# Kernel optimization log

Measured on AMD Instinct MI355X. Metric: run time of the kernel, lower is better.

The kernel has to match this reference:

```python
import jax, jax.numpy as jnp
import numpy as np

B, T, D, H, FF = 4, 2048, 1024, 16, 4096
HD = D // H
EPS = 1e-5


def setup_inputs() -> dict:
    key = jax.random.key(0)
    ks = jax.random.split(key, 10)
    s = lambda k, shape, fan: jax.random.normal(k, shape, jnp.float32) * (1.0 / np.sqrt(fan))
    return {
        "x": jax.random.normal(ks[0], (B, T, D), jnp.float32),
        "ln1_g": jnp.ones((D,), jnp.float32),
        "ln1_b": jnp.zeros((D,), jnp.float32),
        "qkv_w": s(ks[1], (D, 3 * D), D),
        "qkv_b": jnp.zeros((3 * D,), jnp.float32),
        "proj_w": s(ks[2], (D, D), D),
        "proj_b": jnp.zeros((D,), jnp.float32),
        "ln2_g": jnp.ones((D,), jnp.float32),
        "ln2_b": jnp.zeros((D,), jnp.float32),
        "ff1_w": s(ks[3], (D, FF), D),
        "ff1_b": jnp.zeros((FF,), jnp.float32),
        "ff2_w": s(ks[4], (FF, D), FF),
        "ff2_b": jnp.zeros((D,), jnp.float32),
    }


def _layernorm(x, g, b):
    mu = jnp.mean(x, axis=-1, keepdims=True)
    var = jnp.mean(jnp.square(x - mu), axis=-1, keepdims=True)
    return (x - mu) * jax.lax.rsqrt(var + EPS) * g + b


def reference(x, ln1_g, ln1_b, qkv_w, qkv_b, proj_w, proj_b,
              ln2_g, ln2_b, ff1_w, ff1_b, ff2_w, ff2_b):
    # --- attention sublayer ---
    h = _layernorm(x, ln1_g, ln1_b)
    qkv = h @ qkv_w + qkv_b                      # [B,T,3D]
    q, k, v = jnp.split(qkv, 3, axis=-1)
    q = q.reshape(B, T, H, HD).transpose(0, 2, 1, 3)  # [B,H,T,hd]
    k = k.reshape(B, T, H, HD).transpose(0, 2, 1, 3)
    v = v.reshape(B, T, H, HD).transpose(0, 2, 1, 3)
    att = jnp.einsum('bhqd,bhkd->bhqk', q, k) / np.sqrt(HD)
    causal = jnp.tril(jnp.ones((T, T), bool))
    att = jnp.where(causal, att, jnp.finfo(att.dtype).min)
    att = jax.nn.softmax(att, axis=-1)
    out = jnp.einsum('bhqk,bhkd->bhqd', att, v)  # [B,H,T,hd]
    out = out.transpose(0, 2, 1, 3).reshape(B, T, D)
    x = x + out @ proj_w + proj_b
    # --- MLP sublayer ---
    h = _layernorm(x, ln2_g, ln2_b)
    h = jax.nn.gelu(h @ ff1_w + ff1_b, approximate=True)
    x = x + h @ ff2_w + ff2_b
    return x
```

## Files before the change

kernel.cpp:

```cpp
#include <hip/hip_runtime.h>

typedef __attribute__((ext_vector_type(4))) float f32x4;
typedef __attribute__((ext_vector_type(8))) short s16x8;
typedef __attribute__((ext_vector_type(4))) unsigned short u16x4;

#define DEV __device__ __forceinline__

DEV unsigned short f2bf(float f) {
  unsigned int u = __float_as_uint(f);
  return (unsigned short)((u + 0x7FFFu + ((u >> 16) & 1u)) >> 16);
}

DEV float exp2_asm(float x) {
  float r; asm("v_exp_f32 %0, %1" : "=v"(r) : "v"(x)); return r;
}
DEV float rcp_asm(float x) {
  float r; asm("v_rcp_f32 %0, %1" : "=v"(r) : "v"(x)); return r;
}

DEV void gload_lds16(const void* g, void* l) {
  __builtin_amdgcn_global_load_lds(
      (const __attribute__((address_space(1))) unsigned int*)g,
      (__attribute__((address_space(3))) unsigned int*)l, 16, 0, 0);
}

__global__ __launch_bounds__(256) void ln_kernel(
    const float* __restrict__ x, const float* __restrict__ gam,
    const float* __restrict__ bet, unsigned short* __restrict__ o)
{
  const int row = blockIdx.x;
  const int tid = threadIdx.x;
  f32x4 v = *(const f32x4*)(x + (size_t)row * 1024 + tid * 4);
  float s = v[0] + v[1] + v[2] + v[3];
  float s2 = v[0]*v[0] + v[1]*v[1] + v[2]*v[2] + v[3]*v[3];
  #pragma unroll
  for (int m = 1; m < 64; m <<= 1) { s += __shfl_xor(s, m); s2 += __shfl_xor(s2, m); }
  __shared__ float ps[4], ps2[4];
  const int wid = tid >> 6, lane = tid & 63;
  if (lane == 0) { ps[wid] = s; ps2[wid] = s2; }
  __syncthreads();
  s = ps[0] + ps[1] + ps[2] + ps[3];
  s2 = ps2[0] + ps2[1] + ps2[2] + ps2[3];
  const float mu = s * (1.0f / 1024.0f);
  const float rstd = rsqrtf(s2 * (1.0f / 1024.0f) - mu * mu + 1e-5f);
  f32x4 g4 = *(const f32x4*)(gam + tid * 4);
  f32x4 b4 = *(const f32x4*)(bet + tid * 4);
  u16x4 ov;
  #pragma unroll
  for (int j = 0; j < 4; j++) ov[j] = f2bf((v[j] - mu) * rstd * g4[j] + b4[j]);
  *(u16x4*)(o + (size_t)row * 1024 + tid * 4) = ov;
}

__global__ __launch_bounds__(256) void transpose_kernel(
    const float* __restrict__ W, unsigned short* __restrict__ WT, int K, int N)
{
  __shared__ float tile[64][65];
  const int n0 = blockIdx.x * 64, k0 = blockIdx.y * 64;
  const int c = threadIdx.x & 63, r0 = threadIdx.x >> 6;
  #pragma unroll
  for (int r = r0; r < 64; r += 4)
    tile[r][c] = W[(size_t)(k0 + r) * N + n0 + c];
  __syncthreads();
  #pragma unroll
  for (int r = r0; r < 64; r += 4)
    WT[(size_t)(n0 + r) * K + k0 + c] = f2bf(tile[c][r]);
}

template <int MODE>
__global__ __launch_bounds__(512) void gemm8_kernel(
    const unsigned short* __restrict__ A, const unsigned short* __restrict__ WT,
    const float* __restrict__ bias, const float* resid, void* outp,
    int M, int N, int K)
{
  __shared__ unsigned short lds[3 * 24576];
  const int tid = threadIdx.x;
  const int lane = tid & 63, wid = tid >> 6;
  const int l15 = lane & 15, l4 = lane >> 4;
  const int wm = wid >> 2, wn = wid & 3;
  const int tiles_n = N >> 8;
  const int cpx = gridDim.x >> 3;
  const int id = (blockIdx.x & 7) * cpx + (blockIdx.x >> 3);
  const int bm = id / tiles_n, bn = id % tiles_n;
  const int NT = K >> 6;

  const int srow = tid >> 3;
  const int scol = ((tid & 7) ^ (srow & 7)) * 8;
  const unsigned short* Asrc = A  + (size_t)(bm * 128 + srow) * K + scol;
  const unsigned short* Bsrc = WT + (size_t)(bn * 256 + srow) * K + scol;
  const size_t j64 = (size_t)64 * K;
  const int dwave = wid * 1024;

#define STAGE(t_, ss_) do { \
    char* base_ = (char*)lds + (ss_) * 49152 + dwave; \
    const unsigned short* sA_ = Asrc + (size_t)(t_) * 64; \
    const unsigned short* sB_ = Bsrc + (size_t)(t_) * 64; \
    gload_lds16(sA_,            base_); \
    gload_lds16(sA_ + j64,      base_ + 8192); \
    gload_lds16(sB_,            base_ + 16384); \
    gload_lds16(sB_ + j64,      base_ + 16384 + 8192); \
    gload_lds16(sB_ + 2 * j64,  base_ + 16384 + 16384); \
    gload_lds16(sB_ + 3 * j64,  base_ + 16384 + 24576); \
  } while (0)

  f32x4 acc[4][4] = {};

  const int arow0 = wm * 64 + l15;
  const int brow0 = wn * 64 + l15;
  const int cswz = l15 & 7;

  STAGE(0, 0);
  STAGE(1, 1);
  asm volatile("s_waitcnt vmcnt(6)" ::: "memory");
  __builtin_amdgcn_s_barrier();

  int cs = 0, ss = 2;
  for (int t = 0; t < NT; ++t) {
    const unsigned short* sa = lds + cs * 24576;
    const unsigned short* sb = sa + 8192;
    s16x8 af[4][2], bf[4][2];
    #pragma unroll
    for (int mf = 0; mf < 4; ++mf)
      #pragma unroll
      for (int ks = 0; ks < 2; ++ks)
        af[mf][ks] = *(const s16x8*)&sa[(arow0 + mf * 16) * 64 + (((ks * 4 + l4) ^ cswz) * 8)];
    #pragma unroll
    for (int nf = 0; nf < 4; ++nf)
      #pragma unroll
      for (int ks = 0; ks < 2; ++ks)
        bf[nf][ks] = *(const s16x8*)&sb[(brow0 + nf * 16) * 64 + (((ks * 4 + l4) ^ cswz) * 8)];
    if (t + 2 < NT) STAGE(t + 2, ss);
    __builtin_amdgcn_s_setprio(1);
    #pragma unroll
    for (int mf = 0; mf < 4; ++mf)
      #pragma unroll
      for (int nf = 0; nf < 4; ++nf)
        #pragma unroll
        for (int ks = 0; ks < 2; ++ks)
          acc[mf][nf] = __builtin_amdgcn_mfma_f32_16x16x32_bf16(
              af[mf][ks], bf[nf][ks], acc[mf][nf], 0, 0, 0);
    __builtin_amdgcn_s_setprio(0);
    if (t + 2 < NT)      { asm volatile("s_waitcnt vmcnt(6)" ::: "memory"); }
    else if (t + 1 < NT) { asm volatile("s_waitcnt vmcnt(0)" ::: "memory"); }
    __builtin_amdgcn_s_barrier();
    cs = (cs == 2) ? 0 : cs + 1;
    ss = (ss == 2) ? 0 : ss + 1;
  }
#undef STAGE

  #pragma unroll
  for (int nf = 0; nf < 4; nf++) {
    const int col = bn * 256 + wn * 64 + nf * 16 + l15;
    const float bv = bias[col];
    #pragma unroll
    for (int mf = 0; mf < 4; mf++) {
      #pragma unroll
      for (int r = 0; r < 4; r++) {
        const int row = bm * 128 + wm * 64 + mf * 16 + l4 * 4 + r;
        const size_t off = (size_t)row * N + col;
        float v = acc[mf][nf][r] + bv;
        if (MODE == 1) {
          ((float*)outp)[off] = v + resid[off];
        } else if (MODE == 2) {
          const float u = v + 0.044715f * v * v * v;
          const float e = exp2_asm(-2.3022010f * u);
          ((unsigned short*)outp)[off] = f2bf(v * rcp_asm(1.0f + e));
        } else {
          ((unsigned short*)outp)[off] = f2bf(v);
        }
      }
    }
  }
}

struct AttnState {
  f32x4 o[4];
  float m, l;
};

DEV void attn_tile(const s16x8* qf, const unsigned short* Ks,
                   const unsigned short* Vt, unsigned short* Pw,
                   AttnState& st, int kv0, int qg, int l15, int l4, bool need_mask)
{
  f32x4 sa[4];
  #pragma unroll
  for (int cb = 0; cb < 4; cb++) sa[cb] = (f32x4){0.f, 0.f, 0.f, 0.f};
  __builtin_amdgcn_s_setprio(1);
  #pragma unroll
  for (int ks = 0; ks < 2; ++ks) {
    #pragma unroll
    for (int cb = 0; cb < 4; cb++) {
      const int kvr = cb * 16 + l15;
      s16x8 bk = *(const s16x8*)&Ks[kvr * 64 + ((ks * 32 + l4 * 8) ^ ((kvr & 7) << 3))];
      sa[cb] = __builtin_amdgcn_mfma_f32_16x16x32_bf16(bk, qf[ks], sa[cb], 0, 0, 0);
    }
  }
  __builtin_amdgcn_s_setprio(0);
  float mx = -3.0e38f;
  const int thr = qg - kv0 - l4 * 4;
  #pragma unroll
  for (int cb = 0; cb < 4; cb++)
    #pragma unroll
    for (int r = 0; r < 4; r++) {
      float sv = sa[cb][r] * 0.18033688f;
      if (need_mask && (cb * 16 + r > thr)) sv = -3.0e38f;
      sa[cb][r] = sv;
      mx = fmaxf(mx, sv);
    }
  mx = fmaxf(mx, __shfl_xor(mx, 16));
  mx = fmaxf(mx, __shfl_xor(mx, 32));
  const bool skip = __all(mx <= st.m + 11.5f);
  const float mnew = skip ? st.m : fmaxf(st.m, mx);
  float rsum = 0.f;
  #pragma unroll
  for (int cb = 0; cb < 4; cb++) {
    u16x4 pw;
    #pragma unroll
    for (int r = 0; r < 4; r++) {
      const float p = exp2_asm(sa[cb][r] - mnew);
      rsum += p;
      pw[r] = f2bf(p);
    }
    *(u16x4*)&Pw[l15 * 64 + ((cb * 16 + l4 * 4) ^ ((l15 & 7) << 3))] = pw;
  }
  rsum += __shfl_xor(rsum, 16);
  rsum += __shfl_xor(rsum, 32);
  if (skip) {
    st.l += rsum;
  } else {
    const float alpha = exp2_asm(st.m - mnew);
    st.l = st.l * alpha + rsum;
    st.m = mnew;
    #pragma unroll
    for (int r = 0; r < 4; r++) {
      const float ar = __shfl(alpha, l4 * 4 + r);
      #pragma unroll
      for (int cb = 0; cb < 4; cb++) st.o[cb][r] *= ar;
    }
  }
  asm volatile("s_waitcnt lgkmcnt(0)" ::: "memory");
  __builtin_amdgcn_s_setprio(1);
  #pragma unroll
  for (int ks = 0; ks < 2; ++ks) {
    s16x8 pa = *(const s16x8*)&Pw[l15 * 64 + ((ks * 32 + l4 * 8) ^ ((l15 & 7) << 3))];
    #pragma unroll
    for (int cb = 0; cb < 4; cb++) {
      const int d = cb * 16 + l15;
      s16x8 vf = *(const s16x8*)&Vt[d * 64 + ((ks * 32 + l4 * 8) ^ (((d >> 2) & 7) << 3))];
      st.o[cb] = __builtin_amdgcn_mfma_f32_16x16x32_bf16(pa, vf, st.o[cb], 0, 0, 0);
    }
  }
  __builtin_amdgcn_s_setprio(0);
}

DEV void attn_write(unsigned short* orow, const AttnState& st, int l15, int l4) {
  const float invl = rcp_asm(st.l);
  #pragma unroll
  for (int r = 0; r < 4; r++) {
    const float ir = __shfl(invl, l4 * 4 + r);
    #pragma unroll
    for (int cb = 0; cb < 4; cb++)
      orow[(l4 * 4 + r) * 1024 + cb * 16 + l15] = f2bf(st.o[cb][r] * ir);
  }
}

__global__ __launch_bounds__(256) void attn_kernel(
    const unsigned short* __restrict__ qkv, unsigned short* __restrict__ outb)
{
  __shared__ unsigned short Ks[2][64 * 64];
  __shared__ unsigned short Vt[64 * 64];
  __shared__ unsigned short Ps[2][4][16 * 64];
  const int pid = blockIdx.x;
  const int qA = pid, qB = 31 - pid;
  const int bh = blockIdx.y;
  const int b = bh >> 4, h = bh & 15;
  const int tid = threadIdx.x, lane = tid & 63, wid = tid >> 6;
  const int l15 = lane & 15, l4 = lane >> 4;
  const size_t base = (size_t)b * 2048 * 3072 + (size_t)h * 64;
  const unsigned short* Qb = qkv + base;
  const unsigned short* Kb = qkv + base + 1024;
  const unsigned short* Vb = qkv + base + 2048;

  s16x8 qfA[2], qfB[2];
  {
    const unsigned short* qr = Qb + (size_t)(qA * 64 + wid * 16 + l15) * 3072 + l4 * 8;
    qfA[0] = *(const s16x8*)qr;
    qfA[1] = *(const s16x8*)(qr + 32);
    qr = Qb + (size_t)(qB * 64 + wid * 16 + l15) * 3072 + l4 * 8;
    qfB[0] = *(const s16x8*)qr;
    qfB[1] = *(const s16x8*)(qr + 32);
  }

  u16x4 vv[4];
  #pragma unroll
  for (int it = 0; it < 4; ++it) {
    const int cc = tid + 256 * it;
    vv[it] = *(const u16x4*)(Vb + (size_t)(cc >> 4) * 3072 + (cc & 15) * 4);
  }
  #pragma unroll
  for (int s = 0; s < 2; ++s) {
    const int c = s * 256 + tid;
    const int kv = c >> 3;
    const int dsrc = ((c & 7) * 8) ^ ((kv & 7) << 3);
    gload_lds16(Kb + (size_t)kv * 3072 + dsrc, &Ks[0][(size_t)(c & ~63) * 8]);
  }

  AttnState sA, sB;
  #pragma unroll
  for (int cb = 0; cb < 4; cb++) {
    sA.o[cb] = (f32x4){0.f, 0.f, 0.f, 0.f};
    sB.o[cb] = (f32x4){0.f, 0.f, 0.f, 0.f};
  }
  sA.m = -1e30f; sA.l = 0.f; sB.m = -1e30f; sB.l = 0.f;
  const int qgA = qA * 64 + wid * 16 + l15;
  const int qgB = qB * 64 + wid * 16 + l15;

  for (int kvb = 0; kvb <= qB; ++kvb) {
    const int cur = kvb & 1;
    const int kv0 = kvb * 64;
    __builtin_amdgcn_s_barrier();
    asm volatile("s_waitcnt vmcnt(2)" ::: "memory");
    #pragma unroll
    for (int it = 0; it < 4; ++it) {
      const int cc = tid + 256 * it;
      const int vkv = cc >> 4;
      const int vd = (cc & 15) * 4;
      #pragma unroll
      for (int j = 0; j < 4; j++) {
        const int d = vd + j;
        Vt[d * 64 + (vkv ^ (((d >> 2) & 7) << 3))] = vv[it][j];
      }
    }
    if (kvb < qB) {
      #pragma unroll
      for (int it = 0; it < 4; ++it) {
        const int cc = tid + 256 * it;
        vv[it] = *(const u16x4*)(Vb + (size_t)((kvb + 1) * 64 + (cc >> 4)) * 3072 + (cc & 15) * 4);
      }
      asm volatile("s_waitcnt vmcnt(4)" ::: "memory");
    } else {
      asm volatile("s_waitcnt vmcnt(0)" ::: "memory");
    }
    asm volatile("s_waitcnt lgkmcnt(0)" ::: "memory");
    __builtin_amdgcn_s_barrier();
    if (kvb < qB) {
      #pragma unroll
      for (int s = 0; s < 2; ++s) {
        const int c = s * 256 + tid;
        const int kv = c >> 3;
        const int dsrc = ((c & 7) * 8) ^ ((kv & 7) << 3);
        gload_lds16(Kb + (size_t)((kvb + 1) * 64 + kv) * 3072 + dsrc,
                    &Ks[cur ^ 1][(size_t)(c & ~63) * 8]);
      }
    }
    if (kvb <= qA)
      attn_tile(qfA, Ks[cur], Vt, Ps[0][wid], sA, kv0, qgA, l15, l4,
                kv0 + 63 > qA * 64 + wid * 16);
    attn_tile(qfB, Ks[cur], Vt, Ps[1][wid], sB, kv0, qgB, l15, l4,
              kv0 + 63 > qB * 64 + wid * 16);
  }
  attn_write(outb + ((size_t)b * 2048 + qA * 64 + wid * 16) * 1024 + h * 64, sA, l15, l4);
  attn_write(outb + ((size_t)b * 2048 + qB * 64 + wid * 16) * 1024 + h * 64, sB, l15, l4);
}

extern "C" void kernel_launch(void* const* d_in, const int* in_sizes, int n_in,
                              void* d_out, int out_size, void* d_ws, size_t ws_size,
                              hipStream_t stream) {
  const float* x      = (const float*)d_in[0];
  const float* ln1_g  = (const float*)d_in[1];
  const float* ln1_b  = (const float*)d_in[2];
  const float* qkv_w  = (const float*)d_in[3];
  const float* qkv_b  = (const float*)d_in[4];
  const float* proj_w = (const float*)d_in[5];
  const float* proj_b = (const float*)d_in[6];
  const float* ln2_g  = (const float*)d_in[7];
  const float* ln2_b  = (const float*)d_in[8];
  const float* ff1_w  = (const float*)d_in[9];
  const float* ff1_b  = (const float*)d_in[10];
  const float* ff2_w  = (const float*)d_in[11];
  const float* ff2_b  = (const float*)d_in[12];
  float* out = (float*)d_out;

  char* ws = (char*)d_ws;
  size_t off = 0;
  unsigned short* wbuf   = (unsigned short*)(ws + off); off += (size_t)4096 * 1024 * 2;
  unsigned short* hbuf   = (unsigned short*)(ws + off); off += (size_t)8192 * 1024 * 2;
  unsigned short* qkvbuf = (unsigned short*)(ws + off); off += (size_t)8192 * 3072 * 2;
  unsigned short* gbuf   = (unsigned short*)(ws + off);

  ln_kernel<<<8192, 256, 0, stream>>>(x, ln1_g, ln1_b, hbuf);
  transpose_kernel<<<dim3(3072 / 64, 1024 / 64), 256, 0, stream>>>(qkv_w, wbuf, 1024, 3072);
  gemm8_kernel<0><<<dim3(64 * 12), 512, 0, stream>>>(hbuf, wbuf, qkv_b, nullptr, qkvbuf,
                                                     8192, 3072, 1024);
  attn_kernel<<<dim3(16, 64), 256, 0, stream>>>(qkvbuf, hbuf);
  transpose_kernel<<<dim3(1024 / 64, 1024 / 64), 256, 0, stream>>>(proj_w, wbuf, 1024, 1024);
  gemm8_kernel<1><<<dim3(64 * 4), 512, 0, stream>>>(hbuf, wbuf, proj_b, x, out,
                                                    8192, 1024, 1024);
  ln_kernel<<<8192, 256, 0, stream>>>(out, ln2_g, ln2_b, hbuf);
  transpose_kernel<<<dim3(4096 / 64, 1024 / 64), 256, 0, stream>>>(ff1_w, wbuf, 1024, 4096);
  gemm8_kernel<2><<<dim3(64 * 16), 512, 0, stream>>>(hbuf, wbuf, ff1_b, nullptr, gbuf,
                                                     8192, 4096, 1024);
  transpose_kernel<<<dim3(1024 / 64, 4096 / 64), 256, 0, stream>>>(ff2_w, wbuf, 4096, 1024);
  gemm8_kernel<1><<<dim3(64 * 4), 512, 0, stream>>>(gbuf, wbuf, ff2_b, out, out,
                                                    8192, 1024, 4096);
}
```

Measured before the change: 455.1 us.

## Fuse paired query-tile attention to share K/V LDS fragment loads

Merges the two per-query-block attention tile calls into one routine that loads each K and V fragment from LDS once and feeds both query blocks' MFMAs, interleaving their independent work. It also changes the V-transpose LDS swizzle function to a different XOR pattern, applied consistently on write and read. The aim is to halve LDS reads for K/V and give the scheduler more independent MFMA chains, at the cost of higher register pressure from two score accumulators live at once and a divergence-free doA predicate.

```diff
diff --git a/kernel.cpp b/kernel.cpp
--- a/kernel.cpp
+++ b/kernel.cpp
@@ -177,24 +177,11 @@
   float m, l;
 };
 
-DEV void attn_tile(const s16x8* qf, const unsigned short* Ks,
-                   const unsigned short* Vt, unsigned short* Pw,
-                   AttnState& st, int kv0, int qg, int l15, int l4, bool need_mask)
-{
-  f32x4 sa[4];
-  #pragma unroll
-  for (int cb = 0; cb < 4; cb++) sa[cb] = (f32x4){0.f, 0.f, 0.f, 0.f};
-  __builtin_amdgcn_s_setprio(1);
-  #pragma unroll
-  for (int ks = 0; ks < 2; ++ks) {
-    #pragma unroll
-    for (int cb = 0; cb < 4; cb++) {
-      const int kvr = cb * 16 + l15;
-      s16x8 bk = *(const s16x8*)&Ks[kvr * 64 + ((ks * 32 + l4 * 8) ^ ((kvr & 7) << 3))];
-      sa[cb] = __builtin_amdgcn_mfma_f32_16x16x32_bf16(bk, qf[ks], sa[cb], 0, 0, 0);
-    }
-  }
-  __builtin_amdgcn_s_setprio(0);
+DEV int vt_f(int d) { return ((d >> 2) & 3) | ((d & 1) << 2); }
+
+DEV void attn_softmax(f32x4* sa, AttnState& st, unsigned short* Pw,
+                      int kv0, int qg, int l15, int l4, bool need_mask)
+{
   float mx = -3.0e38f;
   const int thr = qg - kv0 - l4 * 4;
   #pragma unroll
@@ -237,16 +224,48 @@
       for (int cb = 0; cb < 4; cb++) st.o[cb][r] *= ar;
     }
   }
+}
+
+DEV void attn_tile2(const s16x8* qfA, const s16x8* qfB,
+                    const unsigned short* Ks, const unsigned short* Vt,
+                    unsigned short* PwA, unsigned short* PwB,
+                    AttnState& sA, AttnState& sB, int kv0,
+                    int qgA, int qgB, int l15, int l4,
+                    bool maskA, bool maskB, bool doA)
+{
+  f32x4 saA[4], saB[4];
+  #pragma unroll
+  for (int cb = 0; cb < 4; cb++) {
+    saA[cb] = (f32x4){0.f, 0.f, 0.f, 0.f};
+    saB[cb] = (f32x4){0.f, 0.f, 0.f, 0.f};
+  }
+  __builtin_amdgcn_s_setprio(1);
+  #pragma unroll
+  for (int ks = 0; ks < 2; ++ks) {
+    #pragma unroll
+    for (int cb = 0; cb < 4; cb++) {
+      const int kvr = cb * 16 + l15;
+      s16x8 bk = *(const s16x8*)&Ks[kvr * 64 + ((ks * 32 + l4 * 8) ^ ((kvr & 7) << 3))];
+      if (doA) saA[cb] = __builtin_amdgcn_mfma_f32_16x16x32_bf16(bk, qfA[ks], saA[cb], 0, 0, 0);
+      saB[cb] = __builtin_amdgcn_mfma_f32_16x16x32_bf16(bk, qfB[ks], saB[cb], 0, 0, 0);
+    }
+  }
+  __builtin_amdgcn_s_setprio(0);
+  if (doA) attn_softmax(saA, sA, PwA, kv0, qgA, l15, l4, maskA);
+  attn_softmax(saB, sB, PwB, kv0, qgB, l15, l4, maskB);
   asm volatile("s_waitcnt lgkmcnt(0)" ::: "memory");
   __builtin_amdgcn_s_setprio(1);
   #pragma unroll
   for (int ks = 0; ks < 2; ++ks) {
-    s16x8 pa = *(const s16x8*)&Pw[l15 * 64 + ((ks * 32 + l4 * 8) ^ ((l15 & 7) << 3))];
+    s16x8 paA, paB;
+    if (doA) paA = *(const s16x8*)&PwA[l15 * 64 + ((ks * 32 + l4 * 8) ^ ((l15 & 7) << 3))];
+    paB = *(const s16x8*)&PwB[l15 * 64 + ((ks * 32 + l4 * 8) ^ ((l15 & 7) << 3))];
     #pragma unroll
     for (int cb = 0; cb < 4; cb++) {
       const int d = cb * 16 + l15;
-      s16x8 vf = *(const s16x8*)&Vt[d * 64 + ((ks * 32 + l4 * 8) ^ (((d >> 2) & 7) << 3))];
-      st.o[cb] = __builtin_amdgcn_mfma_f32_16x16x32_bf16(pa, vf, st.o[cb], 0, 0, 0);
+      s16x8 vf = *(const s16x8*)&Vt[d * 64 + ((ks * 32 + l4 * 8) ^ (vt_f(d) << 3))];
+      if (doA) sA.o[cb] = __builtin_amdgcn_mfma_f32_16x16x32_bf16(paA, vf, sA.o[cb], 0, 0, 0);
+      sB.o[cb] = __builtin_amdgcn_mfma_f32_16x16x32_bf16(paB, vf, sB.o[cb], 0, 0, 0);
     }
   }
   __builtin_amdgcn_s_setprio(0);
@@ -327,7 +346,7 @@
       #pragma unroll
       for (int j = 0; j < 4; j++) {
         const int d = vd + j;
-        Vt[d * 64 + (vkv ^ (((d >> 2) & 7) << 3))] = vv[it][j];
+        Vt[d * 64 + (vkv ^ (vt_f(d) << 3))] = vv[it][j];
       }
     }
     if (kvb < qB) {
@@ -352,11 +371,11 @@
                     &Ks[cur ^ 1][(size_t)(c & ~63) * 8]);
       }
     }
-    if (kvb <= qA)
-      attn_tile(qfA, Ks[cur], Vt, Ps[0][wid], sA, kv0, qgA, l15, l4,
-                kv0 + 63 > qA * 64 + wid * 16);
-    attn_tile(qfB, Ks[cur], Vt, Ps[1][wid], sB, kv0, qgB, l15, l4,
-              kv0 + 63 > qB * 64 + wid * 16);
+    attn_tile2(qfA, qfB, Ks[cur], Vt, Ps[0][wid], Ps[1][wid], sA, sB,
+               kv0, qgA, qgB, l15, l4,
+               kv0 + 63 > qA * 64 + wid * 16,
+               kv0 + 63 > qB * 64 + wid * 16,
+               kvb <= qA);
   }
   attn_write(outb + ((size_t)b * 2048 + qA * 64 + wid * 16) * 1024 + h * 64, sA, l15, l4);
   attn_write(outb + ((size_t)b * 2048 + qB * 64 + wid * 16) * 1024 + h * 64, sB, l15, l4);
```

Measured after the change: 484.1 us. 6.4% more time.
